# Optimization experiments

Measured on AMD Instinct MI355X. Metric: run time of the kernel, lower is better.

Reference implementation:

```python
import jax, jax.numpy as jnp
import numpy as np

N_NODES = 50000
N_EDGES = 800000
IN_F = 128
H_F = 128
OUT_F = 128
N_GRAPHS = 128


def setup_inputs() -> dict:
    key = jax.random.key(0)
    ks = jax.random.split(key, 7)
    x = jax.random.normal(ks[0], (N_NODES, IN_F), dtype=jnp.float32)
    edge_index = jax.random.randint(ks[1], (2, N_EDGES), 0, N_NODES, dtype=jnp.int32)
    batch = jnp.sort(jax.random.randint(ks[2], (N_NODES,), 0, N_GRAPHS, dtype=jnp.int32))
    s1 = 1.0 / np.sqrt(IN_F)
    s2 = 1.0 / np.sqrt(H_F)
    W1 = jax.random.uniform(ks[3], (IN_F, H_F), jnp.float32, -s1, s1)
    b1 = jnp.zeros((H_F,), jnp.float32)
    W2 = jax.random.uniform(ks[4], (H_F, OUT_F), jnp.float32, -s2, s2)
    b2 = jnp.zeros((OUT_F,), jnp.float32)
    return {"x": x, "edge_index": edge_index, "batch": batch,
            "W1": W1, "b1": b1, "W2": W2, "b2": b2}


def _gcn_conv(x, W, b, src, dst, n_nodes):
    # PyG GCNConv: out = D^{-1/2} (A + I) D^{-1/2} (x W) + b
    h = x @ W  # [N, out]
    # degree including self-loop
    deg = jax.ops.segment_sum(jnp.ones_like(dst, dtype=h.dtype), dst,
                              num_segments=n_nodes) + 1.0
    dinv = jax.lax.rsqrt(deg)  # [N]
    norm = dinv[src] * dinv[dst]  # [E]
    agg = jax.ops.segment_sum(h[src] * norm[:, None], dst, num_segments=n_nodes)
    # self-loop term has norm dinv[i]^2
    return agg + (dinv * dinv)[:, None] * h + b


def reference(x, edge_index, batch, W1, b1, W2, b2):
    src, dst = edge_index[0], edge_index[1]
    h = jax.nn.relu(_gcn_conv(x, W1, b1, src, dst, N_NODES))
    h = _gcn_conv(h, W2, b2, src, dst, N_NODES)
    # global_add_pool over graphs
    return jax.ops.segment_sum(h, batch, num_segments=N_GRAPHS)
```

## Files before the change

### kernel.cpp

```cpp
#include <hip/hip_runtime.h>
#include <hip/hip_bf16.h>


typedef _Float16 f16x8 __attribute__((ext_vector_type(8)));
typedef float f32x4 __attribute__((ext_vector_type(4)));

#define BCHUNK 4096

static __device__ __forceinline__ float f16lo(unsigned int u) {
    union { unsigned short s; _Float16 h; } c; c.s = (unsigned short)(u & 0xffff);
    return (float)c.h;
}
static __device__ __forceinline__ float f16hi(unsigned int u) {
    union { unsigned short s; _Float16 h; } c; c.s = (unsigned short)(u >> 16);
    return (float)c.h;
}
static __device__ __forceinline__ unsigned int pack2f16(float x, float y) {
    union { unsigned short s; _Float16 h; } a, b;
    a.h = (_Float16)x; b.h = (_Float16)y;
    return (unsigned int)a.s | ((unsigned int)b.s << 16);
}


__global__ __launch_bounds__(256) void bin_hist(const int* __restrict__ ei,
                                                int* __restrict__ counts,
                                                int E, int NB, int NBLK) {
    __shared__ int hist[256];
    int t = threadIdx.x, blk = blockIdx.x;
    for (int b = t; b < NB; b += 256) hist[b] = 0;
    __syncthreads();
    int base = blk * BCHUNK;
    int end = min(E, base + BCHUNK);
    for (int e = base + t; e < end; e += 256)
        atomicAdd(&hist[ei[E + e] >> 8], 1);
    __syncthreads();
    for (int b = t; b < NB; b += 256) counts[b * NBLK + blk] = hist[b];
}

__global__ __launch_bounds__(256) void bin_scatter(const int* __restrict__ ei,
                                                   const int* __restrict__ counts,
                                                   unsigned int* __restrict__ bedges,
                                                   int E, int NB, int NBLK) {
    __shared__ int lcur[256];
    int t = threadIdx.x, blk = blockIdx.x;
    for (int b = t; b < NB; b += 256) lcur[b] = counts[b * NBLK + blk];
    __syncthreads();
    int base = blk * BCHUNK;
    int end = min(E, base + BCHUNK);
    for (int e = base + t; e < end; e += 256) {
        int s = ei[e];
        int d = ei[E + e];
        int pos = atomicAdd(&lcur[d >> 8], 1);
        bedges[pos] = (unsigned int)s | ((unsigned int)(d & 255) << 16);
    }
}

__global__ __launch_bounds__(256) void deg_buckets(const unsigned int* __restrict__ bedges,
                                                   const int* __restrict__ counts,
                                                   int* __restrict__ cnt,
                                                   int E, int N, int NB, int NBLK) {
    __shared__ int lcnt[256];
    int b = blockIdx.x, t = threadIdx.x;
    lcnt[t] = 0;
    __syncthreads();
    int bstart = counts[b * NBLK];
    int bend = (b + 1 < NB) ? counts[(b + 1) * NBLK] : E;
    for (int i = bstart + t; i < bend; i += 256)
        atomicAdd(&lcnt[bedges[i] >> 16], 1);
    __syncthreads();
    int node = (b << 8) + t;
    if (node < N) cnt[node] = lcnt[t];
}

__global__ __launch_bounds__(256) void fill_buckets(const unsigned int* __restrict__ bedges,
                                                    const int* __restrict__ counts,
                                                    const int* __restrict__ row_start,
                                                    const int* __restrict__ cnt,
                                                    int* __restrict__ srcs,
                                                    int E, int N, int NB, int NBLK) {
    __shared__ int lcur[256];
    int b = blockIdx.x, t = threadIdx.x;
    int node = (b << 8) + t;
    lcur[t] = (node < N) ? row_start[node] : 0;
    __syncthreads();
    int bstart = counts[b * NBLK];
    int bend = (b + 1 < NB) ? counts[(b + 1) * NBLK] : E;
    for (int i = bstart + t; i < bend; i += 256) {
        unsigned int p = bedges[i];
        int pos = atomicAdd(&lcur[p >> 16], 1);
        srcs[pos] = (int)(p & 0xffffu);
    }
    if (node < N) {
        int c = cnt[node];
        int e0 = row_start[node] + c;
        int e1 = row_start[node] + ((c + 7) & ~7);
        for (int j = e0; j < e1; j++) srcs[j] = N;
    }
}


__global__ void block_sums(const int* __restrict__ data, int* __restrict__ bsum, int n) {
    __shared__ int s[256];
    int base = blockIdx.x * 1024;
    int t = threadIdx.x;
    int v = 0;
#pragma unroll
    for (int i = 0; i < 4; i++) {
        int idx = base + t * 4 + i;
        if (idx < n) v += data[idx];
    }
    s[t] = v;
    __syncthreads();
    for (int off = 128; off > 0; off >>= 1) {
        if (t < off) s[t] += s[t + off];
        __syncthreads();
    }
    if (t == 0) bsum[blockIdx.x] = s[0];
}

__global__ void block_sums_pad(const int* __restrict__ data, int* __restrict__ bsum, int n) {
    __shared__ int s[256];
    int base = blockIdx.x * 1024;
    int t = threadIdx.x;
    int v = 0;
#pragma unroll
    for (int i = 0; i < 4; i++) {
        int idx = base + t * 4 + i;
        if (idx < n) v += (data[idx] + 7) & ~7;
    }
    s[t] = v;
    __syncthreads();
    for (int off = 128; off > 0; off >>= 1) {
        if (t < off) s[t] += s[t + off];
        __syncthreads();
    }
    if (t == 0) bsum[blockIdx.x] = s[0];
}

__global__ void scan_bsum(int* __restrict__ bsum, int nb) {
    int lane = threadIdx.x & 63;
    int v = (lane < nb) ? bsum[lane] : 0;
    int incl = v;
#pragma unroll
    for (int off = 1; off < 64; off *= 2) {
        int u = __shfl_up(incl, off);
        if (lane >= off) incl += u;
    }
    if (lane < nb) bsum[lane] = incl - v;
}

__global__ void scan_apply(int* __restrict__ data, const int* __restrict__ bsum, int n) {
    __shared__ int s[256];
    int base = blockIdx.x * 1024;
    int t = threadIdx.x;
    int loc[4];
    int v = 0;
#pragma unroll
    for (int i = 0; i < 4; i++) {
        int idx = base + t * 4 + i;
        loc[i] = (idx < n) ? data[idx] : 0;
        v += loc[i];
    }
    s[t] = v;
    __syncthreads();
    for (int off = 1; off < 256; off *= 2) {
        int u = (t >= off) ? s[t - off] : 0;
        __syncthreads();
        s[t] += u;
        __syncthreads();
    }
    int excl = s[t] - v + bsum[blockIdx.x];
#pragma unroll
    for (int i = 0; i < 4; i++) {
        int idx = base + t * 4 + i;
        if (idx < n) { data[idx] = excl; excl += loc[i]; }
    }
}

__global__ void scan_nodes(const int* __restrict__ cnt, const int* __restrict__ bsum,
                           int* __restrict__ row_start, float* __restrict__ dinv, int n) {
    __shared__ int s[256];
    int base = blockIdx.x * 1024;
    int t = threadIdx.x;
    int loc[4], pc[4];
    int v = 0;
#pragma unroll
    for (int i = 0; i < 4; i++) {
        int idx = base + t * 4 + i;
        loc[i] = (idx < n) ? cnt[idx] : 0;
        pc[i] = (loc[i] + 7) & ~7;
        v += pc[i];
    }
    s[t] = v;
    __syncthreads();
    for (int off = 1; off < 256; off *= 2) {
        int u = (t >= off) ? s[t - off] : 0;
        __syncthreads();
        s[t] += u;
        __syncthreads();
    }
    int excl = s[t] - v + bsum[blockIdx.x];
#pragma unroll
    for (int i = 0; i < 4; i++) {
        int idx = base + t * 4 + i;
        if (idx < n) {
            row_start[idx] = excl;
            dinv[idx] = rsqrtf((float)loc[i] + 1.0f);
            excl += pc[i];
        }
    }
}

__global__ void wprep(const float* __restrict__ W, _Float16* __restrict__ wfrag) {
    int idx = blockIdx.x * 256 + threadIdx.x;
    if (idx >= 2048) return;
    int lane = idx & 63;
    int kc = (idx >> 6) & 3;
    int nb = idx >> 8;
    int col = nb * 16 + (lane & 15);
    int krow = kc * 32 + (lane >> 4) * 8;
#pragma unroll
    for (int j = 0; j < 8; j++)
        wfrag[idx * 8 + j] = (_Float16)W[(krow + j) * 128 + col];
}

__global__ __launch_bounds__(256) void gemm_mfma_f32in(const float* __restrict__ A,
                                                       const _Float16* __restrict__ wfrag,
                                                       const float* __restrict__ dinv,
                                                       _Float16* __restrict__ C, int M) {
    __shared__ _Float16 As[128 * 136];
    int t = threadIdx.x;
    int row0 = blockIdx.x * 128;

    const float4* A4 = (const float4*)A;
#pragma unroll
    for (int it = 0; it < 16; it++) {
        int v = it * 256 + t;
        int row = v >> 5;
        int seg = v & 31;
        float4 val = make_float4(0.f, 0.f, 0.f, 0.f);
        if (row0 + row < M) val = A4[(size_t)(row0 + row) * 32 + seg];
        _Float16* p = &As[row * 136 + seg * 4];
        p[0] = (_Float16)val.x; p[1] = (_Float16)val.y;
        p[2] = (_Float16)val.z; p[3] = (_Float16)val.w;
    }
    __syncthreads();

    int wv = t >> 6;
    int lane = t & 63;
    int lrow = lane & 15;
    int lq = lane >> 4;

    f32x4 acc[2][8];
#pragma unroll
    for (int i = 0; i < 2; i++)
#pragma unroll
        for (int j = 0; j < 8; j++) acc[i][j] = (f32x4){0.f, 0.f, 0.f, 0.f};

#pragma unroll
    for (int kc = 0; kc < 4; kc++) {
        int k0 = kc * 32;
        f16x8 a0 = *((const f16x8*)&As[(wv * 32 + lrow) * 136 + k0 + lq * 8]);
        f16x8 a1 = *((const f16x8*)&As[(wv * 32 + 16 + lrow) * 136 + k0 + lq * 8]);
#pragma unroll
        for (int nb = 0; nb < 8; nb++) {
            f16x8 b = ((const f16x8*)wfrag)[(nb * 4 + kc) * 64 + lane];
            acc[0][nb] = __builtin_amdgcn_mfma_f32_16x16x32_f16(a0, b, acc[0][nb], 0, 0, 0);
            acc[1][nb] = __builtin_amdgcn_mfma_f32_16x16x32_f16(a1, b, acc[1][nb], 0, 0, 0);
        }
    }

#pragma unroll
    for (int ti = 0; ti < 2; ti++) {
#pragma unroll
        for (int r = 0; r < 4; r++) {
            int row = row0 + wv * 32 + ti * 16 + lq * 4 + r;
            if (row < M) {
                float dv = dinv[row];
#pragma unroll
                for (int nb = 0; nb < 8; nb++)
                    C[(size_t)row * 128 + nb * 16 + lrow] = (_Float16)(acc[ti][nb][r] * dv);
            }
        }
    }
}

__global__ __launch_bounds__(256) void agg1(const _Float16* __restrict__ hb,
                                            const int* __restrict__ srcs,
                                            const int* __restrict__ row_start,
                                            const int* __restrict__ cnt,
                                            const float* __restrict__ dinv,
                                            const float* __restrict__ bias,
                                            _Float16* __restrict__ ob, int n) {
    int node = blockIdx.x * 4 + (threadIdx.x >> 6);
    if (node >= n) return;
    int lane = threadIdx.x & 63;
    int s0 = row_start[node];
    int c = cnt[node];
    int nit = (c + 7) >> 3;
    float dn = dinv[node];
    const unsigned int* h2 = (const unsigned int*)hb;
    unsigned int hs = h2[(size_t)node * 64 + lane];
    float2 bv = ((const float2*)bias)[lane];
    float ax = 0.f, ay = 0.f, bx = 0.f, by = 0.f;
    const int4* sp = (const int4*)(srcs + s0);
    int4 sa = {}, sb = {};
    if (nit > 0) { sa = sp[0]; sb = sp[1]; }
    for (int it = 0; it < nit; it++) {
        int4 ca = sa, cb = sb;
        int nx = (it + 1 < nit) ? it + 1 : it;
        sa = sp[nx * 2]; sb = sp[nx * 2 + 1];
        unsigned int v0 = h2[(size_t)(unsigned)ca.x * 64 + lane];
        unsigned int v1 = h2[(size_t)(unsigned)ca.y * 64 + lane];
        unsigned int v2 = h2[(size_t)(unsigned)ca.z * 64 + lane];
        unsigned int v3 = h2[(size_t)(unsigned)ca.w * 64 + lane];
        unsigned int v4 = h2[(size_t)(unsigned)cb.x * 64 + lane];
        unsigned int v5 = h2[(size_t)(unsigned)cb.y * 64 + lane];
        unsigned int v6 = h2[(size_t)(unsigned)cb.z * 64 + lane];
        unsigned int v7 = h2[(size_t)(unsigned)cb.w * 64 + lane];
        ax += f16lo(v0); ay += f16hi(v0);
        bx += f16lo(v1); by += f16hi(v1);
        ax += f16lo(v2); ay += f16hi(v2);
        bx += f16lo(v3); by += f16hi(v3);
        ax += f16lo(v4); ay += f16hi(v4);
        bx += f16lo(v5); by += f16hi(v5);
        ax += f16lo(v6); ay += f16hi(v6);
        bx += f16lo(v7); by += f16hi(v7);
    }
    ax += bx + f16lo(hs);
    ay += by + f16hi(hs);
    float ox = fmaxf(fmaf(dn, ax, bv.x), 0.f) * dn;
    float oy = fmaxf(fmaf(dn, ay, bv.y), 0.f) * dn;
    ((unsigned int*)ob)[(size_t)node * 64 + lane] = pack2f16(ox, oy);
}

__global__ __launch_bounds__(256) void agg2_pool(const _Float16* __restrict__ ob,
                                                 const int* __restrict__ srcs,
                                                 const int* __restrict__ row_start,
                                                 const int* __restrict__ cnt,
                                                 const float* __restrict__ dinv,
                                                 const int* __restrict__ batch,
                                                 float* __restrict__ P, int n) {
    __shared__ float red[4][128];
    int wv = threadIdx.x >> 6;
    int lane = threadIdx.x & 63;
    int base = blockIdx.x * 4;
    int node = base + wv;
    const unsigned int* h2 = (const unsigned int*)ob;
    float tx = 0.f, ty = 0.f;
    int g = -1;
    if (node < n) {
        g = batch[node];
        int s0 = row_start[node];
        int c = cnt[node];
        int nit = (c + 7) >> 3;
        float dn = dinv[node];
        unsigned int hs = h2[(size_t)node * 64 + lane];
        float ax = 0.f, ay = 0.f, bx = 0.f, by = 0.f;
        const int4* sp = (const int4*)(srcs + s0);
        int4 sa = {}, sb = {};
        if (nit > 0) { sa = sp[0]; sb = sp[1]; }
        for (int it = 0; it < nit; it++) {
            int4 ca = sa, cb = sb;
            int nx = (it + 1 < nit) ? it + 1 : it;
            sa = sp[nx * 2]; sb = sp[nx * 2 + 1];
            unsigned int v0 = h2[(size_t)(unsigned)ca.x * 64 + lane];
            unsigned int v1 = h2[(size_t)(unsigned)ca.y * 64 + lane];
            unsigned int v2 = h2[(size_t)(unsigned)ca.z * 64 + lane];
            unsigned int v3 = h2[(size_t)(unsigned)ca.w * 64 + lane];
            unsigned int v4 = h2[(size_t)(unsigned)cb.x * 64 + lane];
            unsigned int v5 = h2[(size_t)(unsigned)cb.y * 64 + lane];
            unsigned int v6 = h2[(size_t)(unsigned)cb.z * 64 + lane];
            unsigned int v7 = h2[(size_t)(unsigned)cb.w * 64 + lane];
            ax += f16lo(v0); ay += f16hi(v0);
            bx += f16lo(v1); by += f16hi(v1);
            ax += f16lo(v2); ay += f16hi(v2);
            bx += f16lo(v3); by += f16hi(v3);
            ax += f16lo(v4); ay += f16hi(v4);
            bx += f16lo(v5); by += f16hi(v5);
            ax += f16lo(v6); ay += f16hi(v6);
            bx += f16lo(v7); by += f16hi(v7);
        }
        ax += bx + f16lo(hs);
        ay += by + f16hi(hs);
        tx = dn * ax;
        ty = dn * ay;
    }
    int lastn = min(base + 3, n - 1);
    bool uniform = (base < n) && (batch[base] == batch[lastn]) && (base + 3 < n);
    if (uniform) {
        red[wv][lane * 2 + 0] = tx;
        red[wv][lane * 2 + 1] = ty;
        __syncthreads();
        if (wv == 0) {
            float sx = red[0][lane * 2] + red[1][lane * 2] + red[2][lane * 2] + red[3][lane * 2];
            float sy = red[0][lane * 2 + 1] + red[1][lane * 2 + 1] + red[2][lane * 2 + 1] + red[3][lane * 2 + 1];
            atomicAdd(&P[g * 128 + lane * 2 + 0], sx);
            atomicAdd(&P[g * 128 + lane * 2 + 1], sy);
        }
    } else if (node < n) {
        atomicAdd(&P[g * 128 + lane * 2 + 0], tx);
        atomicAdd(&P[g * 128 + lane * 2 + 1], ty);
    }
}

__global__ __launch_bounds__(128) void gemm_small(const float* __restrict__ P,
                                                  const float* __restrict__ W2,
                                                  const float* __restrict__ b2,
                                                  const int* __restrict__ batch,
                                                  float* __restrict__ out, int n) {
    __shared__ float prow[128];
    int g = blockIdx.x;
    int c = threadIdx.x;
    prow[c] = P[g * 128 + c];
    __syncthreads();
    int lo = 0, hi = n;
    while (lo < hi) { int mid = (lo + hi) >> 1; if (batch[mid] < g) lo = mid + 1; else hi = mid; }
    int start = lo;
    hi = n;
    while (lo < hi) { int mid = (lo + hi) >> 1; if (batch[mid] < g + 1) lo = mid + 1; else hi = mid; }
    float ng = (float)(lo - start);
    float acc = 0.f;
#pragma unroll 8
    for (int k = 0; k < 128; k++) acc = fmaf(prow[k], W2[k * 128 + c], acc);
    out[g * 128 + c] = acc + ng * b2[c];
}

extern "C" void kernel_launch(void* const* d_in, const int* in_sizes, int n_in,
                              void* d_out, int out_size, void* d_ws, size_t ws_size,
                              hipStream_t stream) {
    const float* x  = (const float*)d_in[0];
    const int*   ei = (const int*)d_in[1];
    const int*   batch = (const int*)d_in[2];
    const float* W1 = (const float*)d_in[3];
    const float* b1 = (const float*)d_in[4];
    const float* W2 = (const float*)d_in[5];
    const float* b2 = (const float*)d_in[6];
    float* out = (float*)d_out;

    const int N = in_sizes[2];
    const int E = in_sizes[1] / 2;

    const int NB = (N + 255) >> 8;
    const int NBLK = (E + BCHUNK - 1) / BCHUNK;
    const int ncounts = NB * NBLK;
    const int SRP = E + 7 * N + 16;

    _Float16* hb = (_Float16*)d_ws;
    _Float16* ob = hb + (size_t)(N + 8) * 128;
    int* cnt  = (int*)(ob + (size_t)(N + 8) * 128);
    int* row_start = cnt + N;
    float* dinv    = (float*)(row_start + N);
    int* srcs      = (int*)(dinv + N);
    unsigned int* bedges = (unsigned int*)(srcs + SRP);
    int* counts    = (int*)(bedges + E);
    _Float16* wfrag1 = (_Float16*)(counts + ncounts);
    float* P       = (float*)(wfrag1 + 128 * 128);
    int* bsum      = (int*)(P + 128 * 128);

    const int nbc = (ncounts + 1023) / 1024;
    const int nbn = (N + 1023) / 1024;

    hipMemsetAsync(P, 0, 128 * 128 * sizeof(float), stream);
    hipMemsetAsync(hb + (size_t)N * 128, 0, 128 * sizeof(_Float16), stream);
    hipMemsetAsync(ob + (size_t)N * 128, 0, 128 * sizeof(_Float16), stream);
    wprep<<<8, 256, 0, stream>>>(W1, wfrag1);

    bin_hist<<<NBLK, 256, 0, stream>>>(ei, counts, E, NB, NBLK);
    block_sums<<<nbc, 256, 0, stream>>>(counts, bsum, ncounts);
    scan_bsum<<<1, 64, 0, stream>>>(bsum, nbc);
    scan_apply<<<nbc, 256, 0, stream>>>(counts, bsum, ncounts);
    bin_scatter<<<NBLK, 256, 0, stream>>>(ei, counts, bedges, E, NB, NBLK);
    deg_buckets<<<NB, 256, 0, stream>>>(bedges, counts, cnt, E, N, NB, NBLK);
    block_sums_pad<<<nbn, 256, 0, stream>>>(cnt, bsum, N);
    scan_bsum<<<1, 64, 0, stream>>>(bsum, nbn);
    scan_nodes<<<nbn, 256, 0, stream>>>(cnt, bsum, row_start, dinv, N);
    fill_buckets<<<NB, 256, 0, stream>>>(bedges, counts, row_start, cnt, srcs, E, N, NB, NBLK);

    const int gemm_grid = (N + 127) / 128;

    gemm_mfma_f32in<<<gemm_grid, 256, 0, stream>>>(x, wfrag1, dinv, hb, N);
    agg1<<<(N + 3) / 4, 256, 0, stream>>>(hb, srcs, row_start, cnt, dinv, b1, ob, N);
    agg2_pool<<<(N + 3) / 4, 256, 0, stream>>>(ob, srcs, row_start, cnt, dinv, batch, P, N);
    gemm_small<<<128, 128, 0, stream>>>(P, W2, b2, batch, out, N);
}
```

Before: 232.7 us.

## Fuse preprocessing kernels and compute degrees via global atomics in histogram pass

Merges memsets, weight fragment prep and the bin histogram into one kernel, which now also counts per-node degree with global atomics instead of a separate bucket pass. The two block-sum, bucket-scan and apply stages for the bin counts and the node counts are fused into combined launches. This cuts the launch count and the serialized dependency chain in the CSR build, at the cost of 800K global atomics spread over 50K counters plus one extra memset.

```diff
diff --git a/kernel.cpp b/kernel.cpp
--- a/kernel.cpp
+++ b/kernel.cpp
@@ -21,20 +21,133 @@
     return (unsigned int)a.s | ((unsigned int)b.s << 16);
 }
 
-
-__global__ __launch_bounds__(256) void bin_hist(const int* __restrict__ ei,
-                                                int* __restrict__ counts,
-                                                int E, int NB, int NBLK) {
+__global__ __launch_bounds__(256) void prep0(const int* __restrict__ ei,
+                                             const float* __restrict__ W1,
+                                             _Float16* __restrict__ wfrag,
+                                             float* __restrict__ P,
+                                             _Float16* __restrict__ hb,
+                                             _Float16* __restrict__ ob,
+                                             int* __restrict__ cnt,
+                                             int* __restrict__ counts,
+                                             int E, int N, int NB, int NBLK) {
     __shared__ int hist[256];
     int t = threadIdx.x, blk = blockIdx.x;
+    int gtid = blk * 256 + t;
+    int gstride = gridDim.x * 256;
+
+    for (int i = gtid; i < 128 * 128; i += gstride) P[i] = 0.f;
+    if (gtid < 64) {
+        ((unsigned int*)(hb + (size_t)N * 128))[gtid] = 0u;
+        ((unsigned int*)(ob + (size_t)N * 128))[gtid] = 0u;
+    }
+    if (gtid < 2048) {
+        int lane = gtid & 63, kc = (gtid >> 6) & 3, nb = gtid >> 8;
+        int col = nb * 16 + (lane & 15);
+        int krow = kc * 32 + (lane >> 4) * 8;
+#pragma unroll
+        for (int j = 0; j < 8; j++)
+            wfrag[gtid * 8 + j] = (_Float16)W1[(krow + j) * 128 + col];
+    }
+
     for (int b = t; b < NB; b += 256) hist[b] = 0;
     __syncthreads();
     int base = blk * BCHUNK;
     int end = min(E, base + BCHUNK);
-    for (int e = base + t; e < end; e += 256)
-        atomicAdd(&hist[ei[E + e] >> 8], 1);
+    for (int e = base + t; e < end; e += 256) {
+        int d = ei[E + e];
+        atomicAdd(&hist[d >> 8], 1);
+        atomicAdd(&cnt[d], 1);
+    }
     __syncthreads();
     for (int b = t; b < NB; b += 256) counts[b * NBLK + blk] = hist[b];
+}
+
+__global__ __launch_bounds__(256) void sums2(const int* __restrict__ counts,
+                                             const int* __restrict__ cnt,
+                                             int* __restrict__ bsum,
+                                             int ncounts, int N, int nbc) {
+    __shared__ int s[256];
+    int t = threadIdx.x;
+    bool isA = (int)blockIdx.x < nbc;
+    int blk = isA ? blockIdx.x : blockIdx.x - nbc;
+    int base = blk * 1024;
+    int v = 0;
+#pragma unroll
+    for (int i = 0; i < 4; i++) {
+        int idx = base + t * 4 + i;
+        if (isA) { if (idx < ncounts) v += counts[idx]; }
+        else     { if (idx < N) v += (cnt[idx] + 7) & ~7; }
+    }
+    s[t] = v;
+    __syncthreads();
+    for (int off = 128; off > 0; off >>= 1) {
+        if (t < off) s[t] += s[t + off];
+        __syncthreads();
+    }
+    if (t == 0) bsum[(isA ? 0 : 64) + blk] = s[0];
+}
+
+__global__ void scan2(int* __restrict__ bsum, int nbc, int nbn) {
+    int w = threadIdx.x >> 6, lane = threadIdx.x & 63;
+    int off0 = w ? 64 : 0;
+    int n = w ? nbn : nbc;
+    int v = (lane < n) ? bsum[off0 + lane] : 0;
+    int incl = v;
+#pragma unroll
+    for (int off = 1; off < 64; off *= 2) {
+        int u = __shfl_up(incl, off);
+        if (lane >= off) incl += u;
+    }
+    if (lane < n) bsum[off0 + lane] = incl - v;
+}
+
+__global__ __launch_bounds__(256) void apply2(int* __restrict__ counts,
+                                              const int* __restrict__ cnt,
+                                              int* __restrict__ row_start,
+                                              float* __restrict__ dinv,
+                                              const int* __restrict__ bsum,
+                                              int ncounts, int N, int nbc) {
+    __shared__ int s[256];
+    int t = threadIdx.x;
+    bool isA = (int)blockIdx.x < nbc;
+    int blk = isA ? blockIdx.x : blockIdx.x - nbc;
+    int base = blk * 1024;
+    int loc[4], pc[4];
+    int v = 0;
+#pragma unroll
+    for (int i = 0; i < 4; i++) {
+        int idx = base + t * 4 + i;
+        if (isA) {
+            loc[i] = (idx < ncounts) ? counts[idx] : 0;
+            pc[i] = loc[i];
+        } else {
+            loc[i] = (idx < N) ? cnt[idx] : 0;
+            pc[i] = (loc[i] + 7) & ~7;
+        }
+        v += pc[i];
+    }
+    s[t] = v;
+    __syncthreads();
+    for (int off = 1; off < 256; off *= 2) {
+        int u = (t >= off) ? s[t - off] : 0;
+        __syncthreads();
+        s[t] += u;
+        __syncthreads();
+    }
+    int excl = s[t] - v + bsum[(isA ? 0 : 64) + blk];
+#pragma unroll
+    for (int i = 0; i < 4; i++) {
+        int idx = base + t * 4 + i;
+        if (isA) {
+            if (idx < ncounts) { counts[idx] = excl; excl += pc[i]; }
+        } else {
+            if (idx < N) {
+                row_start[idx] = excl;
+                dinv[idx] = rsqrtf((float)loc[i] + 1.0f);
+                excl += pc[i];
+            }
+        }
+    }
 }
 
 __global__ __launch_bounds__(256) void bin_scatter(const int* __restrict__ ei,
@@ -53,23 +166,6 @@
         int pos = atomicAdd(&lcur[d >> 8], 1);
         bedges[pos] = (unsigned int)s | ((unsigned int)(d & 255) << 16);
     }
-}
-
-__global__ __launch_bounds__(256) void deg_buckets(const unsigned int* __restrict__ bedges,
-                                                   const int* __restrict__ counts,
-                                                   int* __restrict__ cnt,
-                                                   int E, int N, int NB, int NBLK) {
-    __shared__ int lcnt[256];
-    int b = blockIdx.x, t = threadIdx.x;
-    lcnt[t] = 0;
-    __syncthreads();
-    int bstart = counts[b * NBLK];
-    int bend = (b + 1 < NB) ? counts[(b + 1) * NBLK] : E;
-    for (int i = bstart + t; i < bend; i += 256)
-        atomicAdd(&lcnt[bedges[i] >> 16], 1);
-    __syncthreads();
-    int node = (b << 8) + t;
-    if (node < N) cnt[node] = lcnt[t];
 }
 
 __global__ __launch_bounds__(256) void fill_buckets(const unsigned int* __restrict__ bedges,
@@ -98,132 +194,6 @@
     }
 }
 
-
-__global__ void block_sums(const int* __restrict__ data, int* __restrict__ bsum, int n) {
-    __shared__ int s[256];
-    int base = blockIdx.x * 1024;
-    int t = threadIdx.x;
-    int v = 0;
-#pragma unroll
-    for (int i = 0; i < 4; i++) {
-        int idx = base + t * 4 + i;
-        if (idx < n) v += data[idx];
-    }
-    s[t] = v;
-    __syncthreads();
-    for (int off = 128; off > 0; off >>= 1) {
-        if (t < off) s[t] += s[t + off];
-        __syncthreads();
-    }
-    if (t == 0) bsum[blockIdx.x] = s[0];
-}
-
-__global__ void block_sums_pad(const int* __restrict__ data, int* __restrict__ bsum, int n) {
-    __shared__ int s[256];
-    int base = blockIdx.x * 1024;
-    int t = threadIdx.x;
-    int v = 0;
-#pragma unroll
-    for (int i = 0; i < 4; i++) {
-        int idx = base + t * 4 + i;
-        if (idx < n) v += (data[idx] + 7) & ~7;
-    }
-    s[t] = v;
-    __syncthreads();
-    for (int off = 128; off > 0; off >>= 1) {
-        if (t < off) s[t] += s[t + off];
-        __syncthreads();
-    }
-    if (t == 0) bsum[blockIdx.x] = s[0];
-}
-
-__global__ void scan_bsum(int* __restrict__ bsum, int nb) {
-    int lane = threadIdx.x & 63;
-    int v = (lane < nb) ? bsum[lane] : 0;
-    int incl = v;
-#pragma unroll
-    for (int off = 1; off < 64; off *= 2) {
-        int u = __shfl_up(incl, off);
-        if (lane >= off) incl += u;
-    }
-    if (lane < nb) bsum[lane] = incl - v;
-}
-
-__global__ void scan_apply(int* __restrict__ data, const int* __restrict__ bsum, int n) {
-    __shared__ int s[256];
-    int base = blockIdx.x * 1024;
-    int t = threadIdx.x;
-    int loc[4];
-    int v = 0;
-#pragma unroll
-    for (int i = 0; i < 4; i++) {
-        int idx = base + t * 4 + i;
-        loc[i] = (idx < n) ? data[idx] : 0;
-        v += loc[i];
-    }
-    s[t] = v;
-    __syncthreads();
-    for (int off = 1; off < 256; off *= 2) {
-        int u = (t >= off) ? s[t - off] : 0;
-        __syncthreads();
-        s[t] += u;
-        __syncthreads();
-    }
-    int excl = s[t] - v + bsum[blockIdx.x];
-#pragma unroll
-    for (int i = 0; i < 4; i++) {
-        int idx = base + t * 4 + i;
-        if (idx < n) { data[idx] = excl; excl += loc[i]; }
-    }
-}
-
-__global__ void scan_nodes(const int* __restrict__ cnt, const int* __restrict__ bsum,
-                           int* __restrict__ row_start, float* __restrict__ dinv, int n) {
-    __shared__ int s[256];
-    int base = blockIdx.x * 1024;
-    int t = threadIdx.x;
-    int loc[4], pc[4];
-    int v = 0;
-#pragma unroll
-    for (int i = 0; i < 4; i++) {
-        int idx = base + t * 4 + i;
-        loc[i] = (idx < n) ? cnt[idx] : 0;
-        pc[i] = (loc[i] + 7) & ~7;
-        v += pc[i];
-    }
-    s[t] = v;
-    __syncthreads();
-    for (int off = 1; off < 256; off *= 2) {
-        int u = (t >= off) ? s[t - off] : 0;
-        __syncthreads();
-        s[t] += u;
-        __syncthreads();
-    }
-    int excl = s[t] - v + bsum[blockIdx.x];
-#pragma unroll
-    for (int i = 0; i < 4; i++) {
-        int idx = base + t * 4 + i;
-        if (idx < n) {
-            row_start[idx] = excl;
-            dinv[idx] = rsqrtf((float)loc[i] + 1.0f);
-            excl += pc[i];
-        }
-    }
-}
-
-__global__ void wprep(const float* __restrict__ W, _Float16* __restrict__ wfrag) {
-    int idx = blockIdx.x * 256 + threadIdx.x;
-    if (idx >= 2048) return;
-    int lane = idx & 63;
-    int kc = (idx >> 6) & 3;
-    int nb = idx >> 8;
-    int col = nb * 16 + (lane & 15);
-    int krow = kc * 32 + (lane >> 4) * 8;
-#pragma unroll
-    for (int j = 0; j < 8; j++)
-        wfrag[idx * 8 + j] = (_Float16)W[(krow + j) * 128 + col];
-}
-
 __global__ __launch_bounds__(256) void gemm_mfma_f32in(const float* __restrict__ A,
                                                        const _Float16* __restrict__ wfrag,
                                                        const float* __restrict__ dinv,
@@ -240,9 +210,9 @@
         int seg = v & 31;
         float4 val = make_float4(0.f, 0.f, 0.f, 0.f);
         if (row0 + row < M) val = A4[(size_t)(row0 + row) * 32 + seg];
-        _Float16* p = &As[row * 136 + seg * 4];
-        p[0] = (_Float16)val.x; p[1] = (_Float16)val.y;
-        p[2] = (_Float16)val.z; p[3] = (_Float16)val.w;
+        _Float16* pp = &As[row * 136 + seg * 4];
+        pp[0] = (_Float16)val.x; pp[1] = (_Float16)val.y;
+        pp[2] = (_Float16)val.z; pp[3] = (_Float16)val.w;
     }
     __syncthreads();
 
@@ -440,6 +410,7 @@
 
     const int N = in_sizes[2];
     const int E = in_sizes[1] / 2;
+    const int G = out_size / 128;
 
     const int NB = (N + 255) >> 8;
     const int NBLK = (E + BCHUNK - 1) / BCHUNK;
@@ -461,26 +432,16 @@
     const int nbc = (ncounts + 1023) / 1024;
     const int nbn = (N + 1023) / 1024;
 
-    hipMemsetAsync(P, 0, 128 * 128 * sizeof(float), stream);
-    hipMemsetAsync(hb + (size_t)N * 128, 0, 128 * sizeof(_Float16), stream);
-    hipMemsetAsync(ob + (size_t)N * 128, 0, 128 * sizeof(_Float16), stream);
-    wprep<<<8, 256, 0, stream>>>(W1, wfrag1);
-
-    bin_hist<<<NBLK, 256, 0, stream>>>(ei, counts, E, NB, NBLK);
-    block_sums<<<nbc, 256, 0, stream>>>(counts, bsum, ncounts);
-    scan_bsum<<<1, 64, 0, stream>>>(bsum, nbc);
-    scan_apply<<<nbc, 256, 0, stream>>>(counts, bsum, ncounts);
+    hipMemsetAsync(cnt, 0, (size_t)N * sizeof(int), stream);
+    prep0<<<NBLK, 256, 0, stream>>>(ei, W1, wfrag1, P, hb, ob, cnt, counts, E, N, NB, NBLK);
+    sums2<<<nbc + nbn, 256, 0, stream>>>(counts, cnt, bsum, ncounts, N, nbc);
+    scan2<<<1, 128, 0, stream>>>(bsum, nbc, nbn);
+    apply2<<<nbc + nbn, 256, 0, stream>>>(counts, cnt, row_start, dinv, bsum, ncounts, N, nbc);
     bin_scatter<<<NBLK, 256, 0, stream>>>(ei, counts, bedges, E, NB, NBLK);
-    deg_buckets<<<NB, 256, 0, stream>>>(bedges, counts, cnt, E, N, NB, NBLK);
-    block_sums_pad<<<nbn, 256, 0, stream>>>(cnt, bsum, N);
-    scan_bsum<<<1, 64, 0, stream>>>(bsum, nbn);
-    scan_nodes<<<nbn, 256, 0, stream>>>(cnt, bsum, row_start, dinv, N);
     fill_buckets<<<NB, 256, 0, stream>>>(bedges, counts, row_start, cnt, srcs, E, N, NB, NBLK);
 
-    const int gemm_grid = (N + 127) / 128;
-
-    gemm_mfma_f32in<<<gemm_grid, 256, 0, stream>>>(x, wfrag1, dinv, hb, N);
+    gemm_mfma_f32in<<<(N + 127) / 128, 256, 0, stream>>>(x, wfrag1, dinv, hb, N);
     agg1<<<(N + 3) / 4, 256, 0, stream>>>(hb, srcs, row_start, cnt, dinv, b1, ob, N);
     agg2_pool<<<(N + 3) / 4, 256, 0, stream>>>(ob, srcs, row_start, cnt, dinv, batch, P, N);
-    gemm_small<<<128, 128, 0, stream>>>(P, W2, b2, batch, out, N);
-}
+    gemm_small<<<G, 128, 0, stream>>>(P, W2, b2, batch, out, N);
+}
```

Result: slower. 244.4 us (+5.0%).
